# Kernel tuning notes

Measured on AMD Instinct MI355X. Metric: run time of the kernel, lower is better.

## Reference

```python
import jax, jax.numpy as jnp
import numpy as np

BIG = 1e10  # finite stand-in for +inf so logsumexp grads stay clean
ALPHA = 1.0
SIGMA = 10.0
MARGIN = 2.0
NUM_FRAMES = 2048
GAMMA = 0.1


def pairwise_sqdist(x, y):
    # x:[N,d], y:[M,d] -> [N,M] squared euclidean, via expansion (avoids [N,M,d] temp)
    xn = jnp.sum(x * x, axis=-1)[:, None]
    yn = jnp.sum(y * y, axis=-1)[None, :]
    d = xn + yn - 2.0 * (x @ y.T)
    return jnp.maximum(d, 0.0)


def softdtw(D, gamma):
    # Soft-DTW value via anti-diagonal (wavefront) DP. D:[N,M]
    N, M = D.shape
    K = N + M - 1
    k = jnp.arange(K)[:, None]
    i = jnp.arange(N)[None, :]
    j = k - i
    valid = (j >= 0) & (j < M)
    # skewed cost: Dsk[k, i] = D[i, k-i], padded with BIG
    Dsk = jnp.where(valid, D[jnp.clip(i, 0, N - 1), jnp.clip(j, 0, M - 1)], BIG)

    def shift(r):
        return jnp.concatenate([jnp.full((1,), BIG, r.dtype), r[:-1]])

    def step(carry, d_row):
        r2, r1 = carry  # diagonals k-2 and k-1
        diag = shift(r2)          # R[i-1, j-1]
        up = shift(r1)            # R[i-1, j]
        left = r1                 # R[i, j-1]
        stack = jnp.stack([-diag, -up, -left]) / gamma
        smin = -gamma * jax.scipy.special.logsumexp(stack, axis=0)
        r = d_row + smin
        return (r1, r), None

    r_init2 = jnp.full((N,), BIG, D.dtype)
    r_init1 = jnp.full((N,), BIG, D.dtype).at[0].set(D[0, 0])  # diagonal k=0
    (_, r_last), _ = jax.lax.scan(step, (r_init2, r_init1), Dsk[1:])
    return r_last[N - 1]  # R[N-1, M-1]


def softdtw_normalized(x, y, gamma):
    d_xy = softdtw(pairwise_sqdist(x, y), gamma)
    d_xx = softdtw(pairwise_sqdist(x, x), gamma)
    d_yy = softdtw(pairwise_sqdist(y, y), gamma)
    return d_xy - 0.5 * (d_xx + d_yy)


def contrastive_idm(dist, idx, seq_len):
    gx = idx[:, None]
    gy = idx[None, :]
    prob = jax.nn.relu(MARGIN - dist)
    w_orig = 1.0 + (gx - gy) ** 2
    diff = jnp.abs(gx - gy) - SIGMA / seq_len
    neg = diff > 0
    idm = jnp.where(neg, w_orig, 0.0) * prob + jnp.where(neg, 0.0, 1.0) * dist
    return jnp.sum(idm)


def setup_inputs() -> dict:
    key = jax.random.key(0)
    k1, k2 = jax.random.split(key)
    N, D = 2048, 128
    a_emb = jax.random.normal(k1, (1, N, D), dtype=jnp.float32)
    b_emb = jax.random.normal(k2, (1, N, D), dtype=jnp.float32)
    a_idx = jnp.arange(N, dtype=jnp.float32) / N  # normalized frame indices
    b_idx = jnp.arange(N, dtype=jnp.float32) / N
    return {"a_emb": a_emb, "b_emb": b_emb, "a_idx": a_idx, "b_idx": b_idx,
            "a_len": N, "b_len": N}


def reference(a_emb, b_emb, a_idx, b_idx, a_len, b_len):
    x = a_emb[0]  # [N, d]
    y = b_emb[0]
    pos_loss = softdtw_normalized(x, y, GAMMA)
    idm_a = contrastive_idm(pairwise_sqdist(x, x), a_idx, a_len)
    idm_b = contrastive_idm(pairwise_sqdist(y, y), b_idx, b_len)
    total = pos_loss + ALPHA * (idm_a + idm_b)
    return total / NUM_FRAMES
```

## Files before the change

### kernel.cpp

```cpp
#include <hip/hip_runtime.h>

#define NN   2048
#define DIMK 128
#define BIGF 1e10f

#define WS_XN   0
#define WS_YN   2048
#define WS_ACC  4096
#define WS_FLAG 4112
#define WS_GBUF 4352
#define WS_DSK_BYTES 41984
#define LS_TILES 264
#define MAT_BYTES ((size_t)LS_TILES * 512 * 32)

typedef __attribute__((ext_vector_type(4))) float f32x4;
typedef __attribute__((ext_vector_type(2))) float f32x2;
typedef __attribute__((ext_vector_type(8))) short s16x8;

__global__ __launch_bounds__(256) void norms_kernel(const float* __restrict__ X,
                                                    const float* __restrict__ Y,
                                                    float* __restrict__ ws) {
    if (blockIdx.x == 0) {
        if (threadIdx.x < 8) ws[WS_ACC + threadIdx.x] = 0.0f;
        if (threadIdx.x < 3) ((int*)ws)[WS_FLAG + 16 * threadIdx.x] = 0;
    }
    int gw   = (blockIdx.x * 256 + threadIdx.x) >> 6;
    int lane = threadIdx.x & 63;
    const float* src = (gw < NN) ? (X + (size_t)gw * DIMK) : (Y + (size_t)(gw - NN) * DIMK);
    float2 v = *(const float2*)(src + 2 * lane);
    float s = v.x * v.x + v.y * v.y;
    #pragma unroll
    for (int o = 32; o > 0; o >>= 1) s += __shfl_down(s, o);
    if (lane == 0) ws[(gw < NN) ? (WS_XN + gw) : (WS_YN + (gw - NN))] = s;
}

__device__ __forceinline__ unsigned pk_bf16(float a, float b) {
    unsigned r;
    asm("v_cvt_pk_bf16_f32 %0, %1, %2" : "=v"(r) : "v"(a), "v"(b));
    return r;
}

__global__ __launch_bounds__(256) void dist_kernel(const float* __restrict__ Ain,
                                                   const float* __restrict__ Bin,
                                                   const float* __restrict__ aidx,
                                                   const float* __restrict__ bidx,
                                                   float* __restrict__ ws) {
    const int mat = blockIdx.z;
    const float* A = (mat == 2) ? Bin : Ain;
    const float* B = (mat == 0) ? Bin : A;
    const float* an = ws + (mat == 2 ? WS_YN : WS_XN);
    const float* bn = ws + (mat == 1 ? WS_XN : WS_YN);
    const float* idxv = (mat == 0) ? nullptr : (mat == 1 ? aidx : bidx);
    unsigned char* DskB = (unsigned char*)ws + WS_DSK_BYTES + (size_t)mat * MAT_BYTES;
    __shared__ float red[4];

    const int t = threadIdx.x, w = t >> 6, l = t & 63;
    const int i0g = blockIdx.y * 128 + (w >> 1) * 64;
    const int j0g = blockIdx.x * 128 + (w & 1) * 64;
    const int fr = l & 15, fg = l >> 4;

    f32x4 acc[4][4];
    #pragma unroll
    for (int i = 0; i < 4; ++i)
        #pragma unroll
        for (int j = 0; j < 4; ++j) acc[i][j] = 0.0f;

    #pragma unroll
    for (int kb = 0; kb < 4; ++kb) {
        const int k0 = kb * 32 + fg * 8;
        s16x8 af[4], bf[4];
        #pragma unroll
        for (int ti = 0; ti < 4; ++ti) {
            const float* p = A + (size_t)(i0g + ti * 16 + fr) * DIMK + k0;
            float4 v0 = *(const float4*)p;
            float4 v1 = *(const float4*)(p + 4);
            union { unsigned u[4]; s16x8 v; } rr;
            rr.u[0] = pk_bf16(v0.x, v0.y); rr.u[1] = pk_bf16(v0.z, v0.w);
            rr.u[2] = pk_bf16(v1.x, v1.y); rr.u[3] = pk_bf16(v1.z, v1.w);
            af[ti] = rr.v;
        }
        #pragma unroll
        for (int tj = 0; tj < 4; ++tj) {
            const float* p = B + (size_t)(j0g + tj * 16 + fr) * DIMK + k0;
            float4 v0 = *(const float4*)p;
            float4 v1 = *(const float4*)(p + 4);
            union { unsigned u[4]; s16x8 v; } rr;
            rr.u[0] = pk_bf16(v0.x, v0.y); rr.u[1] = pk_bf16(v0.z, v0.w);
            rr.u[2] = pk_bf16(v1.x, v1.y); rr.u[3] = pk_bf16(v1.z, v1.w);
            bf[tj] = rr.v;
        }
        #pragma unroll
        for (int ti = 0; ti < 4; ++ti)
            #pragma unroll
            for (int tj = 0; tj < 4; ++tj)
                acc[ti][tj] = __builtin_amdgcn_mfma_f32_16x16x32_bf16(
                    af[ti], bf[tj], acc[ti][tj], 0, 0, 0);
    }

    float anv[4][4], gxv[4][4], bnv[4], gyv[4];
    #pragma unroll
    for (int ti = 0; ti < 4; ++ti)
        #pragma unroll
        for (int r = 0; r < 4; ++r) {
            int row = i0g + ti * 16 + fg * 4 + r;
            anv[ti][r] = an[row];
            gxv[ti][r] = idxv ? idxv[row] : 0.0f;
        }
    #pragma unroll
    for (int tj = 0; tj < 4; ++tj) {
        int col = j0g + tj * 16 + fr;
        bnv[tj] = bn[col];
        gyv[tj] = idxv ? idxv[col] : 0.0f;
    }

    float lsum = 0.0f;
    #pragma unroll
    for (int ti = 0; ti < 4; ++ti) {
        const int tt = (i0g >> 2) + ti * 4 + fg;
        #pragma unroll
        for (int tj = 0; tj < 4; ++tj) {
            int col = j0g + tj * 16 + fr;
            int ls = col + (tt & 63);
            float dv[4];
            #pragma unroll
            for (int r = 0; r < 4; ++r)
                dv[r] = fmaxf(anv[ti][r] + bnv[tj] - 2.0f * acc[ti][tj][r], 0.0f);
            unsigned pk = __builtin_amdgcn_cvt_pk_fp8_f32(
                fminf(dv[0], 448.0f), fminf(dv[1], 448.0f), 0, false);
            pk = __builtin_amdgcn_cvt_pk_fp8_f32(
                fminf(dv[2], 448.0f), fminf(dv[3], 448.0f), pk, true);
            *(unsigned*)(DskB + ((size_t)(ls >> 3) * 512 + tt) * 32 + (size_t)(ls & 7) * 4) = pk;
            if (idxv) {
                #pragma unroll
                for (int r = 0; r < 4; ++r) {
                    float dd = gxv[ti][r] - gyv[tj];
                    lsum += (fabsf(dd) > 0.0048828125f)
                            ? (1.0f + dd * dd) * fmaxf(2.0f - dv[r], 0.0f)
                            : dv[r];
                }
            }
        }
    }
    if (idxv) {
        #pragma unroll
        for (int o = 32; o > 0; o >>= 1) lsum += __shfl_down(lsum, o);
        if (l == 0) red[w] = lsum;
        __syncthreads();
        if (t == 0) atomicAdd(ws + WS_ACC + 2 + mat, red[0] + red[1] + red[2] + red[3]);
    }
}

#define RLEN   3248
#define ROFF0  464
#define ROFF1  1088
#define L_INTRA 128
#define LAGX   640

#define DTW_CHUNK(DU, DL, RU, RL)                                              \
    {                                                                          \
        {           \
            int lsn = ls0 + 40;                                                \
            int lsc = lsn < 0 ? 0 : (lsn > 2104 ? 2104 : lsn);                 \
            const uint4* pD =                                                  \
                (const uint4*)(DmB + ((size_t)(lsc >> 3) * 512 + ttg) * 32);   \
            *(uint4*)&dbw[DL][0] = pD[0];                                      \
            *(uint4*)&dbw[DL][4] = pD[1];                                      \
        }                                                                      \
        {     \
            int4 ra = *(const int4*)rptr;                                      \
            int4 rb = *(const int4*)(rptr + 4);                                \
            rvi[RL][0] = ra.x; rvi[RL][1] = ra.y;                              \
            rvi[RL][2] = ra.z; rvi[RL][3] = ra.w;                              \
            rvi[RL][4] = rb.x; rvi[RL][5] = rb.y;                              \
            rvi[RL][6] = rb.z; rvi[RL][7] = rb.w;                              \
            rptr += 8;                                                         \
        }                                                                      \
        _Pragma("unroll")                                                      \
        for (int q = 0; q < 8; ++q) {                                          \
            int up_i = __builtin_amdgcn_update_dpp(rvi[RU][q], prevB_i,        \
                                                   0x138, 0xf, 0xf, false);    \
            float up = __int_as_float(up_i);                                   \
            unsigned wv = dbw[DU][q];                                          \
            f32x2 dlo = __builtin_amdgcn_cvt_pk_f32_fp8(wv, false);            \
            f32x2 dhi = __builtin_amdgcn_cvt_pk_f32_fp8(wv, true);             \
            float m0, m1, m2, m3;                                              \
            asm("v_min3_f32 %0, %1, %2, %3" : "=v"(m0) : "v"(diag), "v"(up), "v"(r0)); \
            float n0 = m0 + dlo.x;                                             \
            asm("v_min3_f32 %0, %1, %2, %3" : "=v"(m1) : "v"(r0), "v"(n0), "v"(r1));   \
            float n1 = m1 + dlo.y;                                             \
            asm("v_min3_f32 %0, %1, %2, %3" : "=v"(m2) : "v"(r1), "v"(n1), "v"(r2));   \
            float n2 = m2 + dhi.x;                                             \
            asm("v_min3_f32 %0, %1, %2, %3" : "=v"(m3) : "v"(r2), "v"(n2), "v"(r3));   \
            float n3 = m3 + dhi.y;                                             \
            diag = up; r0 = n0; r1 = n1; r2 = n2; r3 = n3;                     \
            prevB_i = __float_as_int(n3);                                      \
            wptr[q] = n3;                                                      \
        }                                                                      \
        wptr += 8;                                                             \
        ls0  += 8;                                                             \
    }

__global__ __launch_bounds__(320) void dtw_kernel(float* __restrict__ ws) {
    const int mat  = blockIdx.x >> 1;
    const int bsub = blockIdx.x & 1;
    const unsigned char* __restrict__ DmB =
        (const unsigned char*)ws + WS_DSK_BYTES + (size_t)mat * MAT_BYTES;
    int*   flag = (int*)ws + WS_FLAG + 16 * mat;
    float* gbuf = ws + WS_GBUF + 2048 * mat;
    __shared__ float ring[5 * RLEN];
    __shared__ int cnt[8];
    const int t = threadIdx.x;
    for (int i = t; i < 5 * RLEN; i += 320) ring[i] = BIGF;
    if (t < 8) cnt[t] = 0;
    __syncthreads();

    const int w = t >> 6, l = t & 63;
    volatile int* vcnt = cnt;
    const int roff = bsub ? ROFF1 : ROFF0;

    if (w < 4) {
        const int ttg = 256 * bsub + t;
        float r0 = BIGF, r1 = BIGF, r2 = BIGF, r3 = BIGF, diag = BIGF;
        if (bsub == 0 && t == 0) r0 = 0.0f;
        int prevB_i = __float_as_int(BIGF);

        unsigned dbw[6][8];
        int rvi[2][8];
        int ls0 = -(L_INTRA * w + (bsub ? LAGX : 0));
        float*     wptr = ring + (size_t)(w + 1) * RLEN + (ls0 - l + roff);
        const int* rptr = (const int*)(ring + (size_t)w * RLEN + (ls0 + 8 + roff));

        #pragma unroll
        for (int i = 0; i < 5; ++i) {
            int lsn = ls0 + 8 * i;
            int lsc = lsn < 0 ? 0 : (lsn > 2104 ? 2104 : lsn);
            const uint4* pD = (const uint4*)(DmB + ((size_t)(lsc >> 3) * 512 + ttg) * 32);
            *(uint4*)&dbw[i][0] = pD[0]; *(uint4*)&dbw[i][4] = pD[1];
        }
        #pragma unroll
        for (int q = 0; q < 8; ++q) rvi[0][q] = __float_as_int(BIGF);

        const int myR = (2158 + 128 * w + (bsub ? LAGX : 0)) / 48;
        for (int r = 0; r < myR; ++r) {
            if (w > 0)      { while (vcnt[w - 1] < r) {} }
            else if (bsub)  { int need = r - 2; if (need > 52) need = 52;
                              if (need > 0) while (vcnt[4] < need) {} }
            __asm__ volatile("" ::: "memory");
            DTW_CHUNK(0, 5, 0, 1)
            DTW_CHUNK(1, 0, 1, 0)
            DTW_CHUNK(2, 1, 0, 1)
            DTW_CHUNK(3, 2, 1, 0)
            DTW_CHUNK(4, 3, 0, 1)
            DTW_CHUNK(5, 4, 1, 0)
            __asm__ volatile("" ::: "memory");
            if (l == 0) vcnt[w] = r + 1;
        }
        __asm__ volatile("" ::: "memory");
        if (l == 0) vcnt[w] = 999;

        if (bsub == 1 && t == 0) {
            const int RFIN = (2158 + 128 * 3 + LAGX) / 48;
            while (vcnt[3] < RFIN) {}
            __asm__ volatile("" ::: "memory");
            ws[WS_ACC + mat] = ring[4 * RLEN + roff + (NN - 1)];
        }
    } else if (bsub == 0) {
        for (int q = 1; q <= 52; ++q) {
            while (vcnt[3] < q) __builtin_amdgcn_s_sleep(1);
            __asm__ volatile("" ::: "memory");
            int c = 48 * q - 495 + l;
            if (l < 48 && (unsigned)c < 2048u) {
                float v = ring[4 * RLEN + ROFF0 + c];
                __hip_atomic_store(&gbuf[c], v, __ATOMIC_RELAXED,
                                   __HIP_MEMORY_SCOPE_AGENT);
            }
            if (l == 0)
                __hip_atomic_store(flag, q, __ATOMIC_RELEASE,
                                   __HIP_MEMORY_SCOPE_AGENT);
        }
    } else {
        for (int k = 1; k <= 52; ++k) {
            while (__hip_atomic_load(flag, __ATOMIC_ACQUIRE,
                                     __HIP_MEMORY_SCOPE_AGENT) < k)
                __builtin_amdgcn_s_sleep(1);
            int c = 48 * k - 495 + l;
            if (l < 48 && (unsigned)c < 2048u) {
                float v = __hip_atomic_load(&gbuf[c], __ATOMIC_RELAXED,
                                            __HIP_MEMORY_SCOPE_AGENT);
                ring[ROFF1 + c] = v;
            }
            __asm__ volatile("" ::: "memory");
            if (l == 0) vcnt[4] = k;
        }
        __asm__ volatile("" ::: "memory");
        if (l == 0) vcnt[4] = 999;
    }
}

__global__ void final_kernel(const float* __restrict__ ws, float* __restrict__ out) {
    float v = ws[WS_ACC + 0] - 0.5f * (ws[WS_ACC + 1] + ws[WS_ACC + 2])
            + ws[WS_ACC + 3] + ws[WS_ACC + 4];
    out[0] = v * (1.0f / 2048.0f);
}

extern "C" void kernel_launch(void* const* d_in, const int* in_sizes, int n_in,
                              void* d_out, int out_size, void* d_ws, size_t ws_size,
                              hipStream_t stream) {
    (void)in_sizes; (void)n_in; (void)out_size; (void)ws_size;
    const float* a    = (const float*)d_in[0];
    const float* b    = (const float*)d_in[1];
    const float* aidx = (const float*)d_in[2];
    const float* bidx = (const float*)d_in[3];
    float* ws  = (float*)d_ws;
    float* out = (float*)d_out;

    norms_kernel<<<1024, 256, 0, stream>>>(a, b, ws);
    dist_kernel<<<dim3(16, 16, 3), 256, 0, stream>>>(a, b, aidx, bidx, ws);
    dtw_kernel<<<6, 320, 0, stream>>>(ws);
    final_kernel<<<1, 1, 0, stream>>>(ws, out);
}
```

Measured before the change: 154.3 us.

## Split DTW rows into two interleaved 2-row lanes per thread with ring buffers

Each DTW thread now owns two independent 2-row strips (A and B) instead of one 4-row strip, and interleaves their steps to hide the dependency latency of the serial min3/add chain. The skewed FP8 cost layout changes from 4-row/32-byte tiles to 2-row/16-byte tiles to match. Shared memory uses 512-entry wraparound ring rows per strip, with a new back-pressure wait on the downstream wave so the ring is not overrun. This adds more pipeline stages (larger lag) and more inter-wave synchronization, in exchange for more instruction-level parallelism per thread.

```diff
diff --git a/kernel.cpp b/kernel.cpp
--- a/kernel.cpp
+++ b/kernel.cpp
@@ -11,11 +11,13 @@
 #define WS_GBUF 4352
 #define WS_DSK_BYTES 41984
 #define LS_TILES 264
-#define MAT_BYTES ((size_t)LS_TILES * 512 * 32)
+#define MAT_BYTES ((size_t)LS_TILES * 1024 * 16)
 
 typedef __attribute__((ext_vector_type(4))) float f32x4;
 typedef __attribute__((ext_vector_type(2))) float f32x2;
 typedef __attribute__((ext_vector_type(8))) short s16x8;
+typedef __attribute__((ext_vector_type(4))) int i32x4;
+typedef __attribute__((ext_vector_type(4))) unsigned u32x4;
 
 __global__ __launch_bounds__(256) void norms_kernel(const float* __restrict__ X,
                                                     const float* __restrict__ Y,
@@ -116,20 +118,24 @@
     float lsum = 0.0f;
     #pragma unroll
     for (int ti = 0; ti < 4; ++ti) {
-        const int tt = (i0g >> 2) + ti * 4 + fg;
+        const int u0 = (i0g >> 1) + ti * 8 + fg * 2;
         #pragma unroll
         for (int tj = 0; tj < 4; ++tj) {
             int col = j0g + tj * 16 + fr;
-            int ls = col + (tt & 63);
             float dv[4];
             #pragma unroll
             for (int r = 0; r < 4; ++r)
                 dv[r] = fmaxf(anv[ti][r] + bnv[tj] - 2.0f * acc[ti][tj][r], 0.0f);
-            unsigned pk = __builtin_amdgcn_cvt_pk_fp8_f32(
+            int ls_a = col + (u0 & 63);
+            int ls_b = col + ((u0 + 1) & 63);
+            unsigned pa = __builtin_amdgcn_cvt_pk_fp8_f32(
                 fminf(dv[0], 448.0f), fminf(dv[1], 448.0f), 0, false);
-            pk = __builtin_amdgcn_cvt_pk_fp8_f32(
-                fminf(dv[2], 448.0f), fminf(dv[3], 448.0f), pk, true);
-            *(unsigned*)(DskB + ((size_t)(ls >> 3) * 512 + tt) * 32 + (size_t)(ls & 7) * 4) = pk;
+            unsigned pb = __builtin_amdgcn_cvt_pk_fp8_f32(
+                fminf(dv[2], 448.0f), fminf(dv[3], 448.0f), 0, false);
+            *(unsigned short*)(DskB + ((size_t)(ls_a >> 3) * 1024 + u0) * 16
+                               + (size_t)(ls_a & 7) * 2) = (unsigned short)pa;
+            *(unsigned short*)(DskB + ((size_t)(ls_b >> 3) * 1024 + u0 + 1) * 16
+                               + (size_t)(ls_b & 7) * 2) = (unsigned short)pb;
             if (idxv) {
                 #pragma unroll
                 for (int r = 0; r < 4; ++r) {
@@ -150,54 +156,51 @@
     }
 }
 
-#define RLEN   3248
-#define ROFF0  464
-#define ROFF1  1088
-#define L_INTRA 128
-#define LAGX   640
-
-#define DTW_CHUNK(DU, DL, RU, RL)                                              \
+#define RSTR  512
+#define LCOL  136
+#define LAGX  1176
+#define QMAX  64
+
+#define STEP(S, DU, RU, q)                                                     \
     {                                                                          \
-        {           \
-            int lsn = ls0 + 40;                                                \
-            int lsc = lsn < 0 ? 0 : (lsn > 2104 ? 2104 : lsn);                 \
-            const uint4* pD =                                                  \
-                (const uint4*)(DmB + ((size_t)(lsc >> 3) * 512 + ttg) * 32);   \
-            *(uint4*)&dbw[DL][0] = pD[0];                                      \
-            *(uint4*)&dbw[DL][4] = pD[1];                                      \
-        }                                                                      \
-        {     \
-            int4 ra = *(const int4*)rptr;                                      \
-            int4 rb = *(const int4*)(rptr + 4);                                \
-            rvi[RL][0] = ra.x; rvi[RL][1] = ra.y;                              \
-            rvi[RL][2] = ra.z; rvi[RL][3] = ra.w;                              \
-            rvi[RL][4] = rb.x; rvi[RL][5] = rb.y;                              \
-            rvi[RL][6] = rb.z; rvi[RL][7] = rb.w;                              \
-            rptr += 8;                                                         \
-        }                                                                      \
-        _Pragma("unroll")                                                      \
-        for (int q = 0; q < 8; ++q) {                                          \
-            int up_i = __builtin_amdgcn_update_dpp(rvi[RU][q], prevB_i,        \
-                                                   0x138, 0xf, 0xf, false);    \
-            float up = __int_as_float(up_i);                                   \
-            unsigned wv = dbw[DU][q];                                          \
-            f32x2 dlo = __builtin_amdgcn_cvt_pk_f32_fp8(wv, false);            \
-            f32x2 dhi = __builtin_amdgcn_cvt_pk_f32_fp8(wv, true);             \
-            float m0, m1, m2, m3;                                              \
-            asm("v_min3_f32 %0, %1, %2, %3" : "=v"(m0) : "v"(diag), "v"(up), "v"(r0)); \
-            float n0 = m0 + dlo.x;                                             \
-            asm("v_min3_f32 %0, %1, %2, %3" : "=v"(m1) : "v"(r0), "v"(n0), "v"(r1));   \
-            float n1 = m1 + dlo.y;                                             \
-            asm("v_min3_f32 %0, %1, %2, %3" : "=v"(m2) : "v"(r1), "v"(n1), "v"(r2));   \
-            float n2 = m2 + dhi.x;                                             \
-            asm("v_min3_f32 %0, %1, %2, %3" : "=v"(m3) : "v"(r2), "v"(n2), "v"(r3));   \
-            float n3 = m3 + dhi.y;                                             \
-            diag = up; r0 = n0; r1 = n1; r2 = n2; r3 = n3;                     \
-            prevB_i = __float_as_int(n3);                                      \
-            wptr[q] = n3;                                                      \
-        }                                                                      \
-        wptr += 8;                                                             \
-        ls0  += 8;                                                             \
+        int up_i = __builtin_amdgcn_update_dpp(rv##S[RU][(q) >> 2][(q) & 3],   \
+                                               prevB_##S, 0x138, 0xf, 0xf, false); \
+        float up = __int_as_float(up_i);                                       \
+        f32x2 dd = __builtin_amdgcn_cvt_pk_f32_fp8(db##S[DU][(q) >> 1], (q) & 1); \
+        float m0, m1;                                                          \
+        asm("v_min3_f32 %0, %1, %2, %3"                                        \
+            : "=v"(m0) : "v"(diag_##S), "v"(up), "v"(r0_##S));                 \
+        float n0 = m0 + dd.x;                                                  \
+        asm("v_min3_f32 %0, %1, %2, %3"                                        \
+            : "=v"(m1) : "v"(r0_##S), "v"(n0), "v"(r1_##S));                   \
+        float n1 = m1 + dd.y;                                                  \
+        diag_##S = up; r0_##S = n0; r1_##S = n1;                               \
+        prevB_##S = __float_as_int(n1);                                        \
+        *(float*)((char*)ring + wa_##S) = n1;                                  \
+        wa_##S = wbase_##S | ((wa_##S + 4) & 2047);                            \
+    }
+
+#define CHUNK(DU, DL, RU, RL)                                                  \
+    {                                                                          \
+        { int lsn = lsA + 40; int lsc = lsn < 0 ? 0 : (lsn > 2104 ? 2104 : lsn); \
+          dbA[DL] = *(const u32x4*)(DmB + ((size_t)(lsc >> 3) * 1024 + uA) * 16); } \
+        { int lsn = lsB + 40; int lsc = lsn < 0 ? 0 : (lsn > 2104 ? 2104 : lsn); \
+          dbB[DL] = *(const u32x4*)(DmB + ((size_t)(lsc >> 3) * 1024 + uB) * 16); } \
+        { int ro = (lsA + 8) & 511;                                            \
+          rvA[RL][0] = *(const i32x4*)(rdA + ro);                              \
+          rvA[RL][1] = *(const i32x4*)(rdA + ro + 4); }                        \
+        { int ro = (lsB + 8) & 511;                                            \
+          rvB[RL][0] = *(const i32x4*)(rdB + ro);                              \
+          rvB[RL][1] = *(const i32x4*)(rdB + ro + 4); }                        \
+        STEP(A, DU, RU, 0) STEP(B, DU, RU, 0)                                  \
+        STEP(A, DU, RU, 1) STEP(B, DU, RU, 1)                                  \
+        STEP(A, DU, RU, 2) STEP(B, DU, RU, 2)                                  \
+        STEP(A, DU, RU, 3) STEP(B, DU, RU, 3)                                  \
+        STEP(A, DU, RU, 4) STEP(B, DU, RU, 4)                                  \
+        STEP(A, DU, RU, 5) STEP(B, DU, RU, 5)                                  \
+        STEP(A, DU, RU, 6) STEP(B, DU, RU, 6)                                  \
+        STEP(A, DU, RU, 7) STEP(B, DU, RU, 7)                                  \
+        lsA += 8; lsB += 8;                                                    \
     }
 
 __global__ __launch_bounds__(320) void dtw_kernel(float* __restrict__ ws) {
@@ -207,51 +210,60 @@
         (const unsigned char*)ws + WS_DSK_BYTES + (size_t)mat * MAT_BYTES;
     int*   flag = (int*)ws + WS_FLAG + 16 * mat;
     float* gbuf = ws + WS_GBUF + 2048 * mat;
-    __shared__ float ring[5 * RLEN];
+    __shared__ float ring[9 * RSTR];
     __shared__ int cnt[8];
     const int t = threadIdx.x;
-    for (int i = t; i < 5 * RLEN; i += 320) ring[i] = BIGF;
+    for (int i = t; i < 9 * RSTR; i += 320) ring[i] = BIGF;
     if (t < 8) cnt[t] = 0;
     __syncthreads();
 
     const int w = t >> 6, l = t & 63;
     volatile int* vcnt = cnt;
-    const int roff = bsub ? ROFF1 : ROFF0;
 
     if (w < 4) {
-        const int ttg = 256 * bsub + t;
-        float r0 = BIGF, r1 = BIGF, r2 = BIGF, r3 = BIGF, diag = BIGF;
-        if (bsub == 0 && t == 0) r0 = 0.0f;
-        int prevB_i = __float_as_int(BIGF);
-
-        unsigned dbw[6][8];
-        int rvi[2][8];
-        int ls0 = -(L_INTRA * w + (bsub ? LAGX : 0));
-        float*     wptr = ring + (size_t)(w + 1) * RLEN + (ls0 - l + roff);
-        const int* rptr = (const int*)(ring + (size_t)w * RLEN + (ls0 + 8 + roff));
-
+        const int lagA = LCOL * (2 * w) + (bsub ? LAGX : 0);
+        const int lagB = lagA + LCOL;
+        const int uA = 512 * bsub + 128 * w + l;
+        const int uB = uA + 64;
+        int lsA = -lagA, lsB = -lagB;
+        const int* rdA = (const int*)ring + (2 * w) * RSTR;
+        const int* rdB = (const int*)ring + (2 * w + 1) * RSTR;
+        const int wbase_A = (2 * w + 1) * 2048;
+        const int wbase_B = (2 * w + 2) * 2048;
+        int wa_A = wbase_A + (((lsA - l) & 511) << 2);
+        int wa_B = wbase_B + (((lsB - l) & 511) << 2);
+
+        float r0_A = BIGF, r1_A = BIGF, diag_A = BIGF;
+        float r0_B = BIGF, r1_B = BIGF, diag_B = BIGF;
+        int prevB_A = __float_as_int(BIGF), prevB_B = __float_as_int(BIGF);
+        if (bsub == 0 && w == 0 && l == 0) r0_A = 0.0f;
+
+        u32x4 dbA[6], dbB[6];
+        i32x4 rvA[2][2], rvB[2][2];
         #pragma unroll
         for (int i = 0; i < 5; ++i) {
-            int lsn = ls0 + 8 * i;
-            int lsc = lsn < 0 ? 0 : (lsn > 2104 ? 2104 : lsn);
-            const uint4* pD = (const uint4*)(DmB + ((size_t)(lsc >> 3) * 512 + ttg) * 32);
-            *(uint4*)&dbw[i][0] = pD[0]; *(uint4*)&dbw[i][4] = pD[1];
-        }
-        #pragma unroll
-        for (int q = 0; q < 8; ++q) rvi[0][q] = __float_as_int(BIGF);
-
-        const int myR = (2158 + 128 * w + (bsub ? LAGX : 0)) / 48;
+            int lsn = lsA + 8 * i; int lsc = lsn < 0 ? 0 : (lsn > 2104 ? 2104 : lsn);
+            dbA[i] = *(const u32x4*)(DmB + ((size_t)(lsc >> 3) * 1024 + uA) * 16);
+            lsn = lsB + 8 * i; lsc = lsn < 0 ? 0 : (lsn > 2104 ? 2104 : lsn);
+            dbB[i] = *(const u32x4*)(DmB + ((size_t)(lsc >> 3) * 1024 + uB) * 16);
+        }
+        i32x4 bigv;
+        bigv[0] = bigv[1] = bigv[2] = bigv[3] = __float_as_int(BIGF);
+        rvA[0][0] = bigv; rvA[0][1] = bigv; rvB[0][0] = bigv; rvB[0][1] = bigv;
+
+        const int myR = (2111 + lagB + 47) / 48;
         for (int r = 0; r < myR; ++r) {
             if (w > 0)      { while (vcnt[w - 1] < r) {} }
-            else if (bsub)  { int need = r - 2; if (need > 52) need = 52;
+            else if (bsub)  { int need = r - 2; if (need > QMAX) need = QMAX;
                               if (need > 0) while (vcnt[4] < need) {} }
-            __asm__ volatile("" ::: "memory");
-            DTW_CHUNK(0, 5, 0, 1)
-            DTW_CHUNK(1, 0, 1, 0)
-            DTW_CHUNK(2, 1, 0, 1)
-            DTW_CHUNK(3, 2, 1, 0)
-            DTW_CHUNK(4, 3, 0, 1)
-            DTW_CHUNK(5, 4, 1, 0)
+            if (w < 3)      { int k = r - 5; if (k > 0) while (vcnt[w + 1] < k) {} }
+            __asm__ volatile("" ::: "memory");
+            CHUNK(0, 5, 0, 1)
+            CHUNK(1, 0, 1, 0)
+            CHUNK(2, 1, 0, 1)
+            CHUNK(3, 2, 1, 0)
+            CHUNK(4, 3, 0, 1)
+            CHUNK(5, 4, 1, 0)
             __asm__ volatile("" ::: "memory");
             if (l == 0) vcnt[w] = r + 1;
         }
@@ -259,18 +271,18 @@
         if (l == 0) vcnt[w] = 999;
 
         if (bsub == 1 && t == 0) {
-            const int RFIN = (2158 + 128 * 3 + LAGX) / 48;
+            const int RFIN = (2111 + LCOL * 7 + LAGX + 47) / 48;
             while (vcnt[3] < RFIN) {}
             __asm__ volatile("" ::: "memory");
-            ws[WS_ACC + mat] = ring[4 * RLEN + roff + (NN - 1)];
+            ws[WS_ACC + mat] = ring[8 * RSTR + 511];
         }
     } else if (bsub == 0) {
-        for (int q = 1; q <= 52; ++q) {
+        for (int q = 1; q <= QMAX; ++q) {
             while (vcnt[3] < q) __builtin_amdgcn_s_sleep(1);
             __asm__ volatile("" ::: "memory");
-            int c = 48 * q - 495 + l;
+            int c = 48 * q - 1063 + l;
             if (l < 48 && (unsigned)c < 2048u) {
-                float v = ring[4 * RLEN + ROFF0 + c];
+                float v = ring[8 * RSTR + (c & 511)];
                 __hip_atomic_store(&gbuf[c], v, __ATOMIC_RELAXED,
                                    __HIP_MEMORY_SCOPE_AGENT);
             }
@@ -279,15 +291,15 @@
                                    __HIP_MEMORY_SCOPE_AGENT);
         }
     } else {
-        for (int k = 1; k <= 52; ++k) {
+        for (int k = 1; k <= QMAX; ++k) {
             while (__hip_atomic_load(flag, __ATOMIC_ACQUIRE,
                                      __HIP_MEMORY_SCOPE_AGENT) < k)
                 __builtin_amdgcn_s_sleep(1);
-            int c = 48 * k - 495 + l;
+            int c = 48 * k - 1063 + l;
             if (l < 48 && (unsigned)c < 2048u) {
                 float v = __hip_atomic_load(&gbuf[c], __ATOMIC_RELAXED,
                                             __HIP_MEMORY_SCOPE_AGENT);
-                ring[ROFF1 + c] = v;
+                ring[c & 511] = v;
             }
             __asm__ volatile("" ::: "memory");
             if (l == 0) vcnt[4] = k;
```

After: 285.3 us. 1.85x slower.
